# Kernel optimization log

Measured on AMD Instinct MI355X. Metric: run time of the kernel, lower is better.

The kernel has to match this reference:

```python
import math
import jax, jax.numpy as jnp
import numpy as np

B, L, V, E, H, M, P = 2, 2048, 32000, 512, 1024, 256, 4096


def setup_inputs() -> dict:
    key = jax.random.key(0)
    ks = jax.random.split(key, 16)
    def n(k, shape, s=0.02):
        return jax.random.normal(k, shape, jnp.float32) * s
    return {
        "input_ids": jax.random.randint(ks[0], (B, L), 0, V),
        "untied_token_ids": jax.random.permutation(ks[1], V)[:P],
        "emb": n(ks[2], (V, E)),
        "gru_w_ih": n(ks[3], (3 * H, E)),
        "gru_w_hh": n(ks[4], (3 * H, H)),
        "gru_b_ih": jnp.zeros((3 * H,), jnp.float32),
        "gru_b_hh": jnp.zeros((3 * H,), jnp.float32),
        "wq": n(ks[5], (M, H)), "bq": jnp.zeros((M,), jnp.float32),
        "wk": n(ks[6], (M, H)), "bk": jnp.zeros((M,), jnp.float32),
        "wg": n(ks[7], (1, H)), "bg": jnp.zeros((1,), jnp.float32),
        "w_fc": n(ks[8], (4 * E, H)), "b_fc": jnp.zeros((4 * E,), jnp.float32),
        "w_proj": n(ks[9], (E, 4 * E)), "b_proj": jnp.zeros((E,), jnp.float32),
        "output_bias": jnp.zeros((V,), jnp.float32),
        "w_partial": n(ks[10], (P, E)), "b_partial": jnp.zeros((P,), jnp.float32),
        "memory_scale": jnp.asarray(6.0, jnp.float32),
    }


def reference(input_ids, untied_token_ids, emb, gru_w_ih, gru_w_hh, gru_b_ih,
              gru_b_hh, wq, bq, wk, bk, wg, bg, w_fc, b_fc, w_proj, b_proj,
              output_bias, w_partial, b_partial, memory_scale):
    Bv, Lv = input_ids.shape
    Vv, Ev = emb.shape
    Hv = gru_w_hh.shape[1]
    Pv = untied_token_ids.shape[0]

    x = emb[input_ids]                                    # [B,L,E]
    # GRU (PyTorch gate order r,z,n); precompute input projections
    xp = x @ gru_w_ih.T + gru_b_ih                        # [B,L,3H]
    def step(h, xpt):
        hp = h @ gru_w_hh.T + gru_b_hh
        xr, xz, xn = jnp.split(xpt, 3, axis=-1)
        hr, hz, hn = jnp.split(hp, 3, axis=-1)
        r = jax.nn.sigmoid(xr + hr)
        z = jax.nn.sigmoid(xz + hz)
        nn_ = jnp.tanh(xn + r * hn)
        h = (1.0 - z) * nn_ + z * h
        return h, h
    _, states = jax.lax.scan(step, jnp.zeros((Bv, Hv), x.dtype), jnp.swapaxes(xp, 0, 1))
    states = jnp.swapaxes(states, 0, 1)                   # [B,L,H] (dropout=0 / eval)

    head = jnp.square(jax.nn.relu(states @ w_fc.T + b_fc))
    base_feat = head @ w_proj.T + b_proj                  # [B,L,E]
    base_logits = base_feat @ emb.T + output_bias         # [B,L,V]

    q = states @ wq.T + bq
    k = states @ wk.T + bk
    scores = jnp.einsum('bqm,bkm->bqk', q, k) / math.sqrt(q.shape[-1])
    mask = jnp.tril(jnp.ones((Lv, Lv), bool), -1)[None]   # strict causal
    scores = jnp.where(mask, scores, jnp.finfo(scores.dtype).min)
    attn = jax.nn.softmax(scores, axis=-1) * mask
    attn = attn / jnp.maximum(attn.sum(-1, keepdims=True), 1e-6)

    gate = jax.nn.sigmoid(states @ wg.T + bg)             # [B,L,1]
    attn_g = attn * (gate * memory_scale)

    t2p = jnp.full((Vv,), -1, jnp.int32).at[untied_token_ids].set(
        jnp.arange(Pv, dtype=jnp.int32))
    slots = t2p[input_ids]                                # [B,L]
    valid = (slots >= 0).astype(attn.dtype)
    safe = jnp.maximum(slots, 0)
    def scatter_one(a, s, v):                             # a:[L,L] s,v:[L]
        return jnp.zeros((Lv, Pv), a.dtype).at[:, s].add(a * v[None, :])
    mem_partial = jax.vmap(scatter_one)(attn_g, safe, valid)  # [B,L,P]

    total_partial = base_feat @ w_partial.T + b_partial + mem_partial
    return base_logits.at[:, :, untied_token_ids].add(total_partial)
```

## Files before the change

kernel.cpp:

```cpp
#include <hip/hip_runtime.h>
#include <hip/hip_bf16.h>
#include <math.h>

#define CB 2
#define CL 2048
#define CV 32000
#define CE 512
#define CH 1024
#define CM 256
#define CP 4096
#define CBL (CB*CL)
#define CH3 (3*CH)
#define CE4 (4*CE)

typedef __bf16 bf16x8 __attribute__((ext_vector_type(8)));
typedef float  f32x4  __attribute__((ext_vector_type(4)));
typedef unsigned short bfraw;
typedef unsigned int   u32;
typedef unsigned long long u64;

__device__ __forceinline__ bfraw f2bf(float f) {
  u32 u = __float_as_uint(f);
  u = (u + 0x7fffu + ((u >> 16) & 1u)) >> 16;
  return (bfraw)u;
}

__global__ void k_cvt_bf16(const float* __restrict__ s, bfraw* __restrict__ d, int n4) {
  int i = blockIdx.x * 256 + threadIdx.x;
  if (i >= n4) return;
  f32x4 v = ((const f32x4*)s)[i];
  u32 lo = (u32)f2bf(v[0]) | ((u32)f2bf(v[1]) << 16);
  u32 hi = (u32)f2bf(v[2]) | ((u32)f2bf(v[3]) << 16);
  ((uint2*)d)[i] = make_uint2(lo, hi);
}

__global__ void k_gather_x(const float* __restrict__ emb, const int* __restrict__ ids,
                           bfraw* __restrict__ xbf) {
  int i = blockIdx.x * 256 + threadIdx.x;
  int m = i >> 7;
  int c = i & 127;
  long src = (long)ids[m] * CE + c * 4;
  f32x4 v = *(const f32x4*)(emb + src);
  u32 lo = (u32)f2bf(v[0]) | ((u32)f2bf(v[1]) << 16);
  u32 hi = (u32)f2bf(v[2]) | ((u32)f2bf(v[3]) << 16);
  ((uint2*)xbf)[i] = make_uint2(lo, hi);
}

__global__ void k_fill_t2p(int* t2p) {
  int i = blockIdx.x * 256 + threadIdx.x;
  if (i < CV) t2p[i] = -1;
}
__global__ void k_scatter_t2p(const int* __restrict__ untied, int* __restrict__ t2p) {
  int p = blockIdx.x * 256 + threadIdx.x;
  if (p < CP) t2p[untied[p]] = p;
}
__global__ void k_slots(const int* __restrict__ ids, const int* __restrict__ t2p,
                        int* __restrict__ slots) {
  int i = blockIdx.x * 256 + threadIdx.x;
  if (i < CBL) slots[i] = t2p[ids[i]];
}

enum { EPI_F32B = 0, EPI_RELU2 = 1, EPI_BF = 2, EPI_SCORES = 3, EPI_LOGITS = 4 };

template<int EPI>
__global__ __launch_bounds__(256)
void k_gemm(const bfraw* __restrict__ A, const bfraw* __restrict__ Bw,
            const float* __restrict__ bias, float* __restrict__ Cf,
            bfraw* __restrict__ Cb, int K, int N, float scale,
            long sAz, long sBz, long sCz,
            const int* __restrict__ t2p, const float* __restrict__ tp,
            float* __restrict__ outp)
{
  int bm = blockIdx.x, bn = blockIdx.y, z = blockIdx.z;
  if constexpr (EPI == EPI_SCORES) { if (bn > bm) return; }
  const bfraw* Ap = A + (long)z * sAz;
  const bfraw* Bp = Bw + (long)z * sBz;
  int wave = threadIdx.x >> 6, lane = threadIdx.x & 63;
  int lr = lane & 15, lk = lane >> 4;
  int r0 = bm * 128 + (wave >> 1) * 64;
  int c0 = bn * 128 + (wave & 1) * 64;

  f32x4 acc[4][4] = {};
  const bfraw* arow[4];
  const bfraw* brow[4];
#pragma unroll
  for (int i = 0; i < 4; i++) arow[i] = Ap + (long)(r0 + i * 16 + lr) * K + lk * 8;
#pragma unroll
  for (int j = 0; j < 4; j++) brow[j] = Bp + (long)(c0 + j * 16 + lr) * K + lk * 8;

  for (int k0 = 0; k0 < K; k0 += 32) {
    bf16x8 af[4], bf_[4];
#pragma unroll
    for (int i = 0; i < 4; i++) af[i] = *(const bf16x8*)(arow[i] + k0);
#pragma unroll
    for (int j = 0; j < 4; j++) bf_[j] = *(const bf16x8*)(brow[j] + k0);
#pragma unroll
    for (int i = 0; i < 4; i++)
#pragma unroll
      for (int j = 0; j < 4; j++)
        acc[i][j] = __builtin_amdgcn_mfma_f32_16x16x32_bf16(af[i], bf_[j], acc[i][j], 0, 0, 0);
  }

#pragma unroll
  for (int j = 0; j < 4; j++) {
    int n = c0 + j * 16 + lr;
    float bias_v = 0.f;
    if constexpr (EPI != EPI_SCORES) bias_v = bias[n];
    int s = 0;
    if constexpr (EPI == EPI_LOGITS) s = t2p[n];
#pragma unroll
    for (int i = 0; i < 4; i++) {
#pragma unroll
      for (int r = 0; r < 4; r++) {
        int m = r0 + i * 16 + lk * 4 + r;
        float v = acc[i][j][r];
        if constexpr (EPI == EPI_F32B) {
          Cf[(long)m * N + n] = v + bias_v;
        } else if constexpr (EPI == EPI_RELU2) {
          float t = fmaxf(v + bias_v, 0.f);
          Cb[(long)m * N + n] = f2bf(t * t);
        } else if constexpr (EPI == EPI_BF) {
          Cb[(long)m * N + n] = f2bf(v + bias_v);
        } else if constexpr (EPI == EPI_SCORES) {
          Cf[sCz * z + (long)m * N + n] = v * scale;
        } else {
          float vv = v + bias_v;
          if (s >= 0) vv += tp[(long)m * CP + s];
          outp[(long)m * CV + n] = vv;
        }
      }
    }
  }
}

__global__ __launch_bounds__(256)
void k_gru(const float* __restrict__ Whh, const float* __restrict__ bhh,
           const float* __restrict__ xp, float* __restrict__ states,
           bfraw* __restrict__ statesbf, u64* __restrict__ msgq)
{
  __shared__ float wlds[24 * CH];
  __shared__ float hlds[2 * CH];
  __shared__ float out16[16];
  const int wg = blockIdx.x;
  const int tid = threadIdx.x;
  const int j0 = wg * 8;

  for (int idx = tid; idx < 24 * (CH / 4); idx += 256) {
    int ridx = idx >> 8;
    int kc = idx & 255;
    int g = ridx >> 3, jj = ridx & 7;
    ((f32x4*)wlds)[idx] = ((const f32x4*)(Whh + (long)(g * CH + j0 + jj) * CH))[kc];
  }
  const int jj = tid >> 5, part = tid & 31;
  const int chunk = tid >> 1, half = tid & 1;
  float br = 0, bz = 0, bnn = 0;
  if (part == 0) { br = bhh[j0 + jj]; bz = bhh[CH + j0 + jj]; bnn = bhh[2 * CH + j0 + jj]; }
  __syncthreads();

  for (int t = 0; t < CL; t++) {
    float xr0 = 0, xz0 = 0, xn0 = 0, xr1 = 0, xz1 = 0, xn1 = 0;
    if (part == 0) {
      const float* x0 = xp + (long)t * CH3 + (j0 + jj);
      const float* x1 = xp + (long)(CL + t) * CH3 + (j0 + jj);
      xr0 = x0[0]; xz0 = x0[CH]; xn0 = x0[2 * CH];
      xr1 = x1[0]; xz1 = x1[CH]; xn1 = x1[2 * CH];
    }
    if (t == 0) {
      for (int i = tid; i < 2 * CH; i += 256) hlds[i] = 0.f;
      __syncthreads();
    } else {
      const u32 want = (u32)t;
      u64* base = msgq + ((size_t)(t & 1) * 128 + chunk) * 16 + half * 8;
      float* hdst = hlds + half * CH + chunk * 8;
      bool ok;
      do {
        u64 v[8];
#pragma unroll
        for (int q = 0; q < 8; q++)
          v[q] = __hip_atomic_load(base + q, __ATOMIC_RELAXED, __HIP_MEMORY_SCOPE_AGENT);
        ok = true;
#pragma unroll
        for (int q = 0; q < 8; q++) ok &= ((u32)(v[q] >> 32) == want);
#pragma unroll
        for (int q = 0; q < 8; q++) hdst[q] = __uint_as_float((u32)v[q]);
      } while (!__syncthreads_and((int)ok));
    }

    float ar0 = 0, az0 = 0, an0 = 0, ar1 = 0, az1 = 0, an1 = 0;
    const f32x4* wr = (const f32x4*)(wlds + (0 + jj) * CH);
    const f32x4* wz = (const f32x4*)(wlds + (8 + jj) * CH);
    const f32x4* wn = (const f32x4*)(wlds + (16 + jj) * CH);
    const f32x4* h0 = (const f32x4*)hlds;
    const f32x4* h1 = (const f32x4*)(hlds + CH);
#pragma unroll
    for (int u = 0; u < 8; u++) {
      int k4 = part + 32 * u;
      f32x4 vr = wr[k4], vz = wz[k4], vn = wn[k4];
      f32x4 a0 = h0[k4], a1 = h1[k4];
#pragma unroll
      for (int e = 0; e < 4; e++) {
        ar0 += a0[e] * vr[e]; az0 += a0[e] * vz[e]; an0 += a0[e] * vn[e];
        ar1 += a1[e] * vr[e]; az1 += a1[e] * vz[e]; an1 += a1[e] * vn[e];
      }
    }
#pragma unroll
    for (int d = 1; d < 32; d <<= 1) {
      ar0 += __shfl_xor(ar0, d); az0 += __shfl_xor(az0, d); an0 += __shfl_xor(an0, d);
      ar1 += __shfl_xor(ar1, d); az1 += __shfl_xor(az1, d); an1 += __shfl_xor(an1, d);
    }
    if (part == 0) {
      float hr = ar0 + br, hz = az0 + bz, hn = an0 + bnn;
      float r = 1.f / (1.f + __expf(-(xr0 + hr)));
      float z = 1.f / (1.f + __expf(-(xz0 + hz)));
      float nn = tanhf(xn0 + r * hn);
      float hp = hlds[j0 + jj];
      float hnew0 = (1.f - z) * nn + z * hp;

      hr = ar1 + br; hz = az1 + bz; hn = an1 + bnn;
      float r1 = 1.f / (1.f + __expf(-(xr1 + hr)));
      float z1 = 1.f / (1.f + __expf(-(xz1 + hz)));
      float n1 = tanhf(xn1 + r1 * hn);
      float hp1 = hlds[CH + j0 + jj];
      float hnew1 = (1.f - z1) * n1 + z1 * hp1;

      out16[jj] = hnew0; out16[8 + jj] = hnew1;
      long s0 = (long)t * CH + j0 + jj;
      long s1 = (long)(CL + t) * CH + j0 + jj;
      states[s0] = hnew0;         states[s1] = hnew1;
      statesbf[s0] = f2bf(hnew0); statesbf[s1] = f2bf(hnew1);
    }
    __syncthreads();
    if (tid < 16) {
      u64 v = (u64)__float_as_uint(out16[tid]) | ((u64)(u32)(t + 1) << 32);
      __hip_atomic_store(msgq + ((size_t)((t + 1) & 1) * 128 + wg) * 16 + tid, v,
                         __ATOMIC_RELAXED, __HIP_MEMORY_SCOPE_AGENT);
    }
  }
}

__global__ __launch_bounds__(256)
void k_attn(const float* __restrict__ scores, const float* __restrict__ states,
            const float* __restrict__ wgv, const float* __restrict__ bg,
            const float* __restrict__ mscale, const int* __restrict__ slots,
            float* __restrict__ tp)
{
  int row = blockIdx.x;
  int b = row >> 11, i = row & 2047;
  if (i == 0) return;
  __shared__ float mem[CP];
  __shared__ float es[CL];
  __shared__ float red[4];
  int tid = threadIdx.x;
  for (int p = tid; p < CP; p += 256) mem[p] = 0.f;

  float gd = 0.f;
  const float* st = states + (long)row * CH;
  for (int k = tid; k < CH; k += 256) gd += st[k] * wgv[k];

  const float* srow = scores + (long)b * CL * CL + (long)i * CL;
  float mx = -1e30f;
  for (int k = tid; k < i; k += 256) { float v = srow[k]; es[k] = v; mx = fmaxf(mx, v); }

#pragma unroll
  for (int d = 1; d < 64; d <<= 1) { gd += __shfl_xor(gd, d); mx = fmaxf(mx, __shfl_xor(mx, d)); }
  int wv = tid >> 6;
  if ((tid & 63) == 0) red[wv] = mx;
  __syncthreads();
  mx = fmaxf(fmaxf(red[0], red[1]), fmaxf(red[2], red[3]));
  __syncthreads();
  if ((tid & 63) == 0) red[wv] = gd;
  __syncthreads();
  gd = red[0] + red[1] + red[2] + red[3] + bg[0];
  float gate = 1.f / (1.f + __expf(-gd));
  __syncthreads();

  float se = 0.f;
  for (int k = tid; k < i; k += 256) { float e = __expf(es[k] - mx); es[k] = e; se += e; }
#pragma unroll
  for (int d = 1; d < 64; d <<= 1) se += __shfl_xor(se, d);
  if ((tid & 63) == 0) red[wv] = se;
  __syncthreads();
  se = red[0] + red[1] + red[2] + red[3];
  float coef = gate * mscale[0] / fmaxf(se, 1e-6f);
  __syncthreads();

  for (int k = tid; k < i; k += 256) {
    int s = slots[b * CL + k];
    if (s >= 0) atomicAdd(&mem[s], es[k] * coef);
  }
  __syncthreads();
  float* tprow = tp + (long)row * CP;
  for (int p = tid; p < CP; p += 256) tprow[p] += mem[p];
}

extern "C" void kernel_launch(void* const* d_in, const int* in_sizes, int n_in,
                              void* d_out, int out_size, void* d_ws, size_t ws_size,
                              hipStream_t stream)
{
  const int*   ids    = (const int*)d_in[0];
  const int*   untied = (const int*)d_in[1];
  const float* emb    = (const float*)d_in[2];
  const float* w_ih   = (const float*)d_in[3];
  const float* w_hh   = (const float*)d_in[4];
  const float* b_ih   = (const float*)d_in[5];
  const float* b_hh   = (const float*)d_in[6];
  const float* wq     = (const float*)d_in[7];
  const float* bq     = (const float*)d_in[8];
  const float* wk     = (const float*)d_in[9];
  const float* bk     = (const float*)d_in[10];
  const float* wgv    = (const float*)d_in[11];
  const float* bg     = (const float*)d_in[12];
  const float* w_fc   = (const float*)d_in[13];
  const float* b_fc   = (const float*)d_in[14];
  const float* w_proj = (const float*)d_in[15];
  const float* b_proj = (const float*)d_in[16];
  const float* out_b  = (const float*)d_in[17];
  const float* w_part = (const float*)d_in[18];
  const float* b_part = (const float*)d_in[19];
  const float* mscale = (const float*)d_in[20];
  float* out = (float*)d_out;

  char* ws = (char*)d_ws;
  size_t off = 0;
  auto alloc = [&](size_t bytes) -> char* {
    char* p = ws + off; off += (bytes + 255) & ~(size_t)255; return p;
  };
  bfraw* emb_bf    = (bfraw*)alloc((size_t)CV * CE * 2);
  bfraw* wih_bf    = (bfraw*)alloc((size_t)CH3 * CE * 2);
  bfraw* wfc_bf    = (bfraw*)alloc((size_t)CE4 * CH * 2);
  bfraw* wproj_bf  = (bfraw*)alloc((size_t)CE * CE4 * 2);
  bfraw* wpart_bf  = (bfraw*)alloc((size_t)CP * CE * 2);
  bfraw* wq_bf     = (bfraw*)alloc((size_t)CM * CH * 2);
  bfraw* wk_bf     = (bfraw*)alloc((size_t)CM * CH * 2);
  bfraw* x_bf      = (bfraw*)alloc((size_t)CBL * CE * 2);
  float* xp        = (float*)alloc((size_t)CBL * CH3 * 4);
  float* states    = (float*)alloc((size_t)CBL * CH * 4);
  bfraw* states_bf = (bfraw*)alloc((size_t)CBL * CH * 2);
  bfraw* head_bf   = (bfraw*)alloc((size_t)CBL * CE4 * 2);
  bfraw* bfeat_bf  = (bfraw*)alloc((size_t)CBL * CE * 2);
  bfraw* q_bf      = (bfraw*)alloc((size_t)CBL * CM * 2);
  bfraw* k_bf      = (bfraw*)alloc((size_t)CBL * CM * 2);
  float* tp        = (float*)alloc((size_t)CBL * CP * 4);
  int*   t2p       = (int*)alloc((size_t)CV * 4);
  int*   slots     = (int*)alloc((size_t)CBL * 4);
  u64*   msgq      = (u64*)alloc(sizeof(u64) * 2 * 128 * 16);
  float* scores    = xp;
  (void)in_sizes; (void)n_in; (void)out_size; (void)ws_size;

  auto cvt = [&](const float* s, bfraw* d, int n) {
    int n4 = n / 4;
    k_cvt_bf16<<<(n4 + 255) / 256, 256, 0, stream>>>(s, d, n4);
  };
  cvt(emb, emb_bf, CV * CE);
  cvt(w_ih, wih_bf, CH3 * CE);
  cvt(w_fc, wfc_bf, CE4 * CH);
  cvt(w_proj, wproj_bf, CE * CE4);
  cvt(w_part, wpart_bf, CP * CE);
  cvt(wq, wq_bf, CM * CH);
  cvt(wk, wk_bf, CM * CH);
  k_fill_t2p<<<(CV + 255) / 256, 256, 0, stream>>>(t2p);
  k_scatter_t2p<<<CP / 256, 256, 0, stream>>>(untied, t2p);
  k_slots<<<CBL / 256, 256, 0, stream>>>(ids, t2p, slots);
  k_gather_x<<<(CBL * CE / 4) / 256, 256, 0, stream>>>(emb, ids, x_bf);

  k_gemm<EPI_F32B><<<dim3(CBL / 128, CH3 / 128), 256, 0, stream>>>(
      x_bf, wih_bf, b_ih, xp, nullptr, CE, CH3, 1.f, 0, 0, 0, nullptr, nullptr, nullptr);

  k_gru<<<128, 256, 0, stream>>>(w_hh, b_hh, xp, states, states_bf, msgq);

  k_gemm<EPI_RELU2><<<dim3(CBL / 128, CE4 / 128), 256, 0, stream>>>(
      states_bf, wfc_bf, b_fc, nullptr, head_bf, CH, CE4, 1.f, 0, 0, 0, nullptr, nullptr, nullptr);
  k_gemm<EPI_BF><<<dim3(CBL / 128, CE / 128), 256, 0, stream>>>(
      head_bf, wproj_bf, b_proj, nullptr, bfeat_bf, CE4, CE, 1.f, 0, 0, 0, nullptr, nullptr, nullptr);
  k_gemm<EPI_BF><<<dim3(CBL / 128, CM / 128), 256, 0, stream>>>(
      states_bf, wq_bf, bq, nullptr, q_bf, CH, CM, 1.f, 0, 0, 0, nullptr, nullptr, nullptr);
  k_gemm<EPI_BF><<<dim3(CBL / 128, CM / 128), 256, 0, stream>>>(
      states_bf, wk_bf, bk, nullptr, k_bf, CH, CM, 1.f, 0, 0, 0, nullptr, nullptr, nullptr);
  k_gemm<EPI_SCORES><<<dim3(CL / 128, CL / 128, CB), 256, 0, stream>>>(
      q_bf, k_bf, nullptr, scores, nullptr, CM, CL, 0.0625f,
      (long)CL * CM, (long)CL * CM, (long)CL * CL, nullptr, nullptr, nullptr);
  k_gemm<EPI_F32B><<<dim3(CBL / 128, CP / 128), 256, 0, stream>>>(
      bfeat_bf, wpart_bf, b_part, tp, nullptr, CE, CP, 1.f, 0, 0, 0, nullptr, nullptr, nullptr);
  k_attn<<<CBL, 256, 0, stream>>>(scores, states, wgv, bg, mscale, slots, tp);
  k_gemm<EPI_LOGITS><<<dim3(CBL / 128, CV / 128), 256, 0, stream>>>(
      bfeat_bf, emb_bf, out_b, nullptr, nullptr, CE, CV, 1.f, 0, 0, 0, t2p, tp, out);
}
```

Before: 9.898 ms.

## Keep GRU recurrent weights in registers and streamline per-step cross-block sync

The persistent GRU kernel now holds each thread's slice of W_hh in registers instead of LDS and double-buffers the hidden-state LDS array. Each thread polls its own message slots until they are ready, rather than looping over a block-wide __syncthreads_and. Lane 0 of each row publishes the new hidden value straight to the message queue, dropping the out16 staging buffer and one barrier per step. This is meant to cut per-timestep latency on the serial 2048-step recurrence, at the cost of about 96 weight registers per thread.

```diff
diff --git a/kernel.cpp b/kernel.cpp
--- a/kernel.cpp
+++ b/kernel.cpp
@@ -133,31 +133,36 @@
   }
 }
 
-__global__ __launch_bounds__(256)
+__global__ __launch_bounds__(256, 1)
 void k_gru(const float* __restrict__ Whh, const float* __restrict__ bhh,
            const float* __restrict__ xp, float* __restrict__ states,
            bfraw* __restrict__ statesbf, u64* __restrict__ msgq)
 {
-  __shared__ float wlds[24 * CH];
-  __shared__ float hlds[2 * CH];
-  __shared__ float out16[16];
+  __shared__ float hlds[2][2 * CH];
   const int wg = blockIdx.x;
   const int tid = threadIdx.x;
   const int j0 = wg * 8;
-
-  for (int idx = tid; idx < 24 * (CH / 4); idx += 256) {
-    int ridx = idx >> 8;
-    int kc = idx & 255;
-    int g = ridx >> 3, jj = ridx & 7;
-    ((f32x4*)wlds)[idx] = ((const f32x4*)(Whh + (long)(g * CH + j0 + jj) * CH))[kc];
-  }
   const int jj = tid >> 5, part = tid & 31;
   const int chunk = tid >> 1, half = tid & 1;
-  float br = 0, bz = 0, bnn = 0;
-  if (part == 0) { br = bhh[j0 + jj]; bz = bhh[CH + j0 + jj]; bnn = bhh[2 * CH + j0 + jj]; }
+
+  f32x4 wr[8], wz[8], wn[8];
+  {
+    const f32x4* R = (const f32x4*)(Whh + (long)(0 * CH + j0 + jj) * CH);
+    const f32x4* Z = (const f32x4*)(Whh + (long)(1 * CH + j0 + jj) * CH);
+    const f32x4* N = (const f32x4*)(Whh + (long)(2 * CH + j0 + jj) * CH);
+#pragma unroll
+    for (int u = 0; u < 8; u++) {
+      wr[u] = R[part + 32 * u];
+      wz[u] = Z[part + 32 * u];
+      wn[u] = N[part + 32 * u];
+    }
+  }
+  const float br = bhh[j0 + jj], bz = bhh[CH + j0 + jj], bnn = bhh[2 * CH + j0 + jj];
+  for (int i = tid; i < 2 * CH; i += 256) hlds[0][i] = 0.f;
   __syncthreads();
 
   for (int t = 0; t < CL; t++) {
+    const int cur = t & 1;
     float xr0 = 0, xz0 = 0, xn0 = 0, xr1 = 0, xz1 = 0, xn1 = 0;
     if (part == 0) {
       const float* x0 = xp + (long)t * CH3 + (j0 + jj);
@@ -165,42 +170,36 @@
       xr0 = x0[0]; xz0 = x0[CH]; xn0 = x0[2 * CH];
       xr1 = x1[0]; xz1 = x1[CH]; xn1 = x1[2 * CH];
     }
-    if (t == 0) {
-      for (int i = tid; i < 2 * CH; i += 256) hlds[i] = 0.f;
-      __syncthreads();
-    } else {
+    if (t > 0) {
       const u32 want = (u32)t;
-      u64* base = msgq + ((size_t)(t & 1) * 128 + chunk) * 16 + half * 8;
-      float* hdst = hlds + half * CH + chunk * 8;
+      const u64* src = msgq + ((size_t)cur * 128 + chunk) * 16 + half * 8;
+      u64 v[8];
       bool ok;
       do {
-        u64 v[8];
+        ok = true;
 #pragma unroll
         for (int q = 0; q < 8; q++)
-          v[q] = __hip_atomic_load(base + q, __ATOMIC_RELAXED, __HIP_MEMORY_SCOPE_AGENT);
-        ok = true;
+          v[q] = __hip_atomic_load(src + q, __ATOMIC_RELAXED, __HIP_MEMORY_SCOPE_AGENT);
 #pragma unroll
         for (int q = 0; q < 8; q++) ok &= ((u32)(v[q] >> 32) == want);
-#pragma unroll
-        for (int q = 0; q < 8; q++) hdst[q] = __uint_as_float((u32)v[q]);
-      } while (!__syncthreads_and((int)ok));
+      } while (!ok);
+      float* hdst = hlds[cur] + half * CH + chunk * 8;
+#pragma unroll
+      for (int q = 0; q < 8; q++) hdst[q] = __uint_as_float((u32)v[q]);
+      __syncthreads();
     }
 
     float ar0 = 0, az0 = 0, an0 = 0, ar1 = 0, az1 = 0, an1 = 0;
-    const f32x4* wr = (const f32x4*)(wlds + (0 + jj) * CH);
-    const f32x4* wz = (const f32x4*)(wlds + (8 + jj) * CH);
-    const f32x4* wn = (const f32x4*)(wlds + (16 + jj) * CH);
-    const f32x4* h0 = (const f32x4*)hlds;
-    const f32x4* h1 = (const f32x4*)(hlds + CH);
+    const f32x4* h0 = (const f32x4*)(hlds[cur]);
+    const f32x4* h1 = (const f32x4*)(hlds[cur] + CH);
 #pragma unroll
     for (int u = 0; u < 8; u++) {
       int k4 = part + 32 * u;
-      f32x4 vr = wr[k4], vz = wz[k4], vn = wn[k4];
       f32x4 a0 = h0[k4], a1 = h1[k4];
 #pragma unroll
       for (int e = 0; e < 4; e++) {
-        ar0 += a0[e] * vr[e]; az0 += a0[e] * vz[e]; an0 += a0[e] * vn[e];
-        ar1 += a1[e] * vr[e]; az1 += a1[e] * vz[e]; an1 += a1[e] * vn[e];
+        ar0 += a0[e] * wr[u][e]; az0 += a0[e] * wz[u][e]; an0 += a0[e] * wn[u][e];
+        ar1 += a1[e] * wr[u][e]; az1 += a1[e] * wz[u][e]; an1 += a1[e] * wn[u][e];
       }
     }
 #pragma unroll
@@ -213,27 +212,26 @@
       float r = 1.f / (1.f + __expf(-(xr0 + hr)));
       float z = 1.f / (1.f + __expf(-(xz0 + hz)));
       float nn = tanhf(xn0 + r * hn);
-      float hp = hlds[j0 + jj];
+      float hp = hlds[cur][j0 + jj];
       float hnew0 = (1.f - z) * nn + z * hp;
 
       hr = ar1 + br; hz = az1 + bz; hn = an1 + bnn;
       float r1 = 1.f / (1.f + __expf(-(xr1 + hr)));
       float z1 = 1.f / (1.f + __expf(-(xz1 + hz)));
       float n1 = tanhf(xn1 + r1 * hn);
-      float hp1 = hlds[CH + j0 + jj];
+      float hp1 = hlds[cur][CH + j0 + jj];
       float hnew1 = (1.f - z1) * n1 + z1 * hp1;
 
-      out16[jj] = hnew0; out16[8 + jj] = hnew1;
+      u64* dst = msgq + ((size_t)((t + 1) & 1) * 128 + wg) * 16;
+      u64 m0 = (u64)__float_as_uint(hnew0) | ((u64)(u32)(t + 1) << 32);
+      u64 m1 = (u64)__float_as_uint(hnew1) | ((u64)(u32)(t + 1) << 32);
+      __hip_atomic_store(dst + jj, m0, __ATOMIC_RELAXED, __HIP_MEMORY_SCOPE_AGENT);
+      __hip_atomic_store(dst + 8 + jj, m1, __ATOMIC_RELAXED, __HIP_MEMORY_SCOPE_AGENT);
+
       long s0 = (long)t * CH + j0 + jj;
       long s1 = (long)(CL + t) * CH + j0 + jj;
       states[s0] = hnew0;         states[s1] = hnew1;
       statesbf[s0] = f2bf(hnew0); statesbf[s1] = f2bf(hnew1);
-    }
-    __syncthreads();
-    if (tid < 16) {
-      u64 v = (u64)__float_as_uint(out16[tid]) | ((u64)(u32)(t + 1) << 32);
-      __hip_atomic_store(msgq + ((size_t)((t + 1) & 1) * 128 + wg) * 16 + tid, v,
-                         __ATOMIC_RELAXED, __HIP_MEMORY_SCOPE_AGENT);
     }
   }
 }
```

New measurement: 9.850 ms. Within noise of the previous version (-0.5%).
